# Optimization experiments

Hardware: AMD Instinct MI355X
Metric: run time of the kernel (lower is better)

The kernel has to match this reference:

```python
import jax, jax.numpy as jnp
import numpy as np

B, M, D = 16, 100000, 128
OUT = 128  # out_features; in_features = 2*D


def setup_inputs() -> dict:
    key = jax.random.key(0)
    k1, k2, k3, k4 = jax.random.split(key, 4)
    s1 = 1.0 / np.sqrt(2 * D)  # ~ torch Linear default init scale
    s2 = 1.0 / np.sqrt(OUT)
    return {
        "xx_anchor": jax.random.normal(k1, (B, D), dtype=jnp.float32),
        "input": jax.random.normal(k2, (M, D), dtype=jnp.float32),
        "adj": jnp.zeros((1, 1), dtype=jnp.float32),  # densified then unused in forward math
        "W1": jax.random.normal(k3, (OUT, 2 * D), dtype=jnp.float32) * s1,
        "W2": jax.random.normal(k4, (1, OUT), dtype=jnp.float32) * s2,
    }


def reference(xx_anchor, input, adj, W1, W2):
    d = input.shape[1]
    # concat(q_vec, input) @ W1.T  ==  q @ W1[:, :d].T  +  input @ W1[:, d:].T
    # (avoids materializing the [B, m, 2d] concat tensor; same math)
    anchor_part = xx_anchor @ W1[:, :d].T          # [B, out]
    node_part = input @ W1[:, d:].T                # [m, out]
    h = jax.nn.relu(anchor_part[:, None, :] + node_part[None, :, :])  # [B, m, out]
    scores = jnp.einsum('bmo,o->bm', h, W2[0])     # linear2 -> [B, m]
    atten = jax.nn.softmax(scores, axis=1)          # softmax over node dim
    v_vec = jnp.einsum('bm,md->bd', atten, input)   # weighted sum pooling
    return v_vec
```

## Files before the change

kernel.cpp:

```cpp
#include <hip/hip_runtime.h>
#include <hip/hip_bf16.h>
#include <math.h>


typedef __attribute__((ext_vector_type(8))) short bf16x8;
typedef __attribute__((ext_vector_type(4))) float f32x4;

__device__ __forceinline__ short f2bs(float f) {
    __hip_bfloat16 h = __float2bfloat16(f);
    return *reinterpret_cast<short*>(&h);
}
__device__ __forceinline__ float bs2f(ushort u) {
    union { unsigned int i; float f; } v; v.i = ((unsigned)u) << 16; return v.f;
}

__global__ __launch_bounds__(256) void kA(const float* __restrict__ W1,
                                          const float* __restrict__ xx,
                                          ushort* __restrict__ w1b,
                                          float* __restrict__ A) {
    const int bi = blockIdx.x, t = threadIdx.x;
    if (bi < 64) {
        int idx = bi * 256 + t;
        int o = idx >> 7, d = idx & 127;
        w1b[idx] = (ushort)f2bs(W1[o * 256 + 128 + d]);
        return;
    }
    __shared__ float xxs[16 * 132];
    __shared__ float w1s[16 * 132];
    const int og0 = (bi - 64) * 16;
#pragma unroll
    for (int i = 0; i < 2; ++i) {
        int idx = t + 256 * i;
        int r = idx >> 5, c4 = (idx & 31) << 2;
        *(float4*)&xxs[r * 132 + c4] = *(const float4*)&xx[r * 128 + c4];
        *(float4*)&w1s[r * 132 + c4] = *(const float4*)&W1[(og0 + r) * 256 + c4];
    }
    __syncthreads();
    const int ol = t >> 4, b = t & 15;
    float acc = 0.f;
#pragma unroll
    for (int d4 = 0; d4 < 32; ++d4) {
        float4 xv = *(float4*)&xxs[b * 132 + d4 * 4];
        float4 wv = *(float4*)&w1s[ol * 132 + d4 * 4];
        acc += xv.x * wv.x + xv.y * wv.y + xv.z * wv.z + xv.w * wv.w;
    }
    A[b * 128 + og0 + ol] = acc;
}

__global__ __launch_bounds__(256, 3) void kB(
    const float* __restrict__ in, const ushort* __restrict__ w1b,
    const float* __restrict__ W2, const float* __restrict__ A,
    float* __restrict__ lsum_g, ushort* __restrict__ pacc, int M) {
    __shared__ ushort ins[128 * 136];
    __shared__ float As[16 * 128];
    __shared__ ushort pb[16 * 136];

    const int tid = threadIdx.x, bid = blockIdx.x;
    const int m0 = bid * 128;
    const int w = tid >> 6, lane = tid & 63;
    const int c = lane & 15, q = lane >> 4;
    const int lim = (M - m0 < 128) ? (M - m0) : 128;

#pragma unroll
    for (int i = 0; i < 16; ++i) {
        int idx = tid + 256 * i;
        int r = idx >> 5, c4 = (idx & 31) << 2;
        float4 v = make_float4(0.f, 0.f, 0.f, 0.f);
        if (r < lim) v = *(const float4*)&in[(size_t)(m0 + r) * 128 + c4];
        ushort4 u;
        u.x = (ushort)f2bs(v.x); u.y = (ushort)f2bs(v.y);
        u.z = (ushort)f2bs(v.z); u.w = (ushort)f2bs(v.w);
        *(ushort4*)&ins[r * 136 + c4] = u;
    }
#pragma unroll
    for (int i = 0; i < 2; ++i) {
        int idx = tid + 256 * i;
        *(float4*)&As[idx * 4] = *(const float4*)&A[idx * 4];
    }
    __syncthreads();

    const int mbase = w * 32 + c;
    f32x4 acc[2][8];
#pragma unroll
    for (int mt = 0; mt < 2; ++mt)
#pragma unroll
        for (int ot = 0; ot < 8; ++ot) acc[mt][ot] = (f32x4){0.f, 0.f, 0.f, 0.f};
#pragma unroll
    for (int kb = 0; kb < 4; ++kb) {
        bf16x8 bv0 = *(const bf16x8*)&ins[mbase * 136 + kb * 32 + q * 8];
        bf16x8 bv1 = *(const bf16x8*)&ins[(mbase + 16) * 136 + kb * 32 + q * 8];
#pragma unroll
        for (int ot = 0; ot < 8; ++ot) {
            bf16x8 av = *(const bf16x8*)(w1b + (ot * 16 + c) * 128 + kb * 32 + q * 8);
            acc[0][ot] = __builtin_amdgcn_mfma_f32_16x16x32_bf16(av, bv0, acc[0][ot], 0, 0, 0);
            acc[1][ot] = __builtin_amdgcn_mfma_f32_16x16x32_bf16(av, bv1, acc[1][ot], 0, 0, 0);
        }
    }

    f32x4 w2q[8];
#pragma unroll
    for (int ot = 0; ot < 8; ++ot)
        w2q[ot] = *(const f32x4*)&W2[ot * 16 + q * 4];

    const bool mv0 = (w * 32 + c) < lim;
    const bool mv1 = (w * 32 + 16 + c) < lim;
#pragma unroll
    for (int b = 0; b < 16; ++b) {
        float sa0 = 0.f, sa1 = 0.f;
#pragma unroll
        for (int ot = 0; ot < 8; ++ot) {
            f32x4 aq = *(f32x4*)&As[b * 128 + ot * 16 + q * 4];
#pragma unroll
            for (int r = 0; r < 4; ++r) {
                sa0 += fmaxf(acc[0][ot][r] + aq[r], 0.f) * w2q[ot][r];
                sa1 += fmaxf(acc[1][ot][r] + aq[r], 0.f) * w2q[ot][r];
            }
        }
        sa0 += __shfl_xor(sa0, 16, 64);
        sa0 += __shfl_xor(sa0, 32, 64);
        sa1 += __shfl_xor(sa1, 16, 64);
        sa1 += __shfl_xor(sa1, 32, 64);
        if (q == (b & 3)) {
            pb[b * 136 + w * 32 + c]      = (ushort)f2bs(mv0 ? __expf(sa0) : 0.f);
            pb[b * 136 + w * 32 + 16 + c] = (ushort)f2bs(mv1 ? __expf(sa1) : 0.f);
        }
    }
    __syncthreads();

    f32x4 pd[2];
    pd[0] = (f32x4){0.f, 0.f, 0.f, 0.f};
    pd[1] = (f32x4){0.f, 0.f, 0.f, 0.f};
#pragma unroll
    for (int ks = 0; ks < 4; ++ks) {
        bf16x8 pf = *(const bf16x8*)&pb[c * 136 + ks * 32 + q * 8];
#pragma unroll
        for (int t = 0; t < 2; ++t) {
            const int dloc = w * 32 + t * 16 + c;
            bf16x8 bf;
#pragma unroll
            for (int j = 0; j < 8; ++j)
                bf[j] = (short)ins[(ks * 32 + q * 8 + j) * 136 + dloc];
            pd[t] = __builtin_amdgcn_mfma_f32_16x16x32_bf16(pf, bf, pd[t], 0, 0, 0);
        }
    }
#pragma unroll
    for (int t = 0; t < 2; ++t)
#pragma unroll
        for (int r = 0; r < 4; ++r)
            pacc[((size_t)bid * 16 + q * 4 + r) * 128 + w * 32 + t * 16 + c] =
                (ushort)f2bs(pd[t][r]);

    {
        const int bb = tid >> 4, jj = tid & 15;
        const ushort* pr = &pb[bb * 136 + jj * 8];
        float part = 0.f;
#pragma unroll
        for (int j2 = 0; j2 < 8; ++j2) part += bs2f(pr[j2]);
#pragma unroll
        for (int off = 1; off < 16; off <<= 1) part += __shfl_xor(part, off, 64);
        if (jj == 0) lsum_g[bid * 16 + bb] = part;
    }
}

__global__ __launch_bounds__(256) void kC1(
    const float* __restrict__ lsum_g, const ushort* __restrict__ pacc,
    float* __restrict__ pacc2, float* __restrict__ lsum2, int nb) {
    const int b = blockIdx.x >> 4, s = blockIdx.x & 15;
    const int t = threadIdx.x;
    __shared__ float reda[2 * 128];
    __shared__ float redl[2];
    const int cs = (nb + 15) >> 4;
    const int blk0 = s * cs;
    int blk1 = blk0 + cs; if (blk1 > nb) blk1 = nb;
    const int dd = t & 127, h = t >> 7;
    float ac = 0.f, ls = 0.f;
    for (int blk = blk0 + h; blk < blk1; blk += 2) {
        ac += bs2f(pacc[((size_t)blk * 16 + b) * 128 + dd]);
        ls += lsum_g[blk * 16 + b];
    }
    reda[h * 128 + dd] = ac;
    if (dd == 0) redl[h] = ls;
    __syncthreads();
    if (h == 0) {
        pacc2[((size_t)s * 16 + b) * 128 + dd] = reda[dd] + reda[128 + dd];
        if (dd == 0) lsum2[s * 16 + b] = redl[0] + redl[1];
    }
}

__global__ void kFin(const float* __restrict__ pacc2, const float* __restrict__ lsum2,
                     float* __restrict__ out) {
    const int b = blockIdx.x, t = threadIdx.x;
    float ac = 0.f, ls = 0.f;
#pragma unroll
    for (int s = 0; s < 16; ++s) {
        ac += pacc2[((size_t)s * 16 + b) * 128 + t];
        ls += lsum2[s * 16 + b];
    }
    out[b * 128 + t] = ac / ls;
}

extern "C" void kernel_launch(void* const* d_in, const int* in_sizes, int n_in,
                              void* d_out, int out_size, void* d_ws, size_t ws_size,
                              hipStream_t stream) {
    const float* xx = (const float*)d_in[0];
    const float* in = (const float*)d_in[1];
    const float* W1 = (const float*)d_in[3];
    const float* W2 = (const float*)d_in[4];
    float* out = (float*)d_out;

    const int M = in_sizes[1] / 128;
    const int nb = (M + 127) / 128;

    float* ws = (float*)d_ws;
    float* A      = ws;
    float* lsum_g = A + 2048;
    float* pacc2  = lsum_g + (size_t)nb * 16;
    float* lsum2  = pacc2 + 256 * 128;
    ushort* w1b   = (ushort*)(lsum2 + 256);
    ushort* pacc  = w1b + 16384;

    kA  <<<72, 256, 0, stream>>>(W1, xx, w1b, A);
    kB  <<<nb, 256, 0, stream>>>(in, w1b, W2, A, lsum_g, pacc, M);
    kC1 <<<256, 256, 0, stream>>>(lsum_g, pacc, pacc2, lsum2, nb);
    kFin<<<16, 128, 0, stream>>>(pacc2, lsum2, out);
}
```

Before: 146.3 us.

## Fuse cross-block reduction into main kernel via atomics and last-block finalize

Replaces the per-block bf16 partial outputs and two follow-up reduction kernels with float atomicAdds into a global accumulator, plus a last-block-done counter that writes the final normalized output. It also rewrites relu as 0.5*(x+|x|), hoisting the x*w2 term out of the per-batch loop so the inner loop does abs instead of max. The intent is to cut two kernel launches and the pacc write/read traffic. The cost is heavy atomic contention on 2048 addresses from ~780 blocks, and summation order is no longer deterministic.

```diff
diff --git a/kernel.cpp b/kernel.cpp
--- a/kernel.cpp
+++ b/kernel.cpp
@@ -17,7 +17,10 @@
 __global__ __launch_bounds__(256) void kA(const float* __restrict__ W1,
                                           const float* __restrict__ xx,
                                           ushort* __restrict__ w1b,
-                                          float* __restrict__ A) {
+                                          float* __restrict__ A,
+                                          float* __restrict__ acc_g,
+                                          float* __restrict__ lsum_acc,
+                                          int* __restrict__ counter) {
     const int bi = blockIdx.x, t = threadIdx.x;
     if (bi < 64) {
         int idx = bi * 256 + t;
@@ -25,6 +28,14 @@
         w1b[idx] = (ushort)f2bs(W1[o * 256 + 128 + d]);
         return;
     }
+    if (bi == 72) {
+        for (int i = t; i < 2064; i += 256) {
+            if (i < 2048) acc_g[i] = 0.f;
+            else          lsum_acc[i - 2048] = 0.f;
+        }
+        if (t == 0) *counter = 0;
+        return;
+    }
     __shared__ float xxs[16 * 132];
     __shared__ float w1s[16 * 132];
     const int og0 = (bi - 64) * 16;
@@ -50,7 +61,8 @@
 __global__ __launch_bounds__(256, 3) void kB(
     const float* __restrict__ in, const ushort* __restrict__ w1b,
     const float* __restrict__ W2, const float* __restrict__ A,
-    float* __restrict__ lsum_g, ushort* __restrict__ pacc, int M) {
+    float* __restrict__ acc_g, float* __restrict__ lsum_acc,
+    int* __restrict__ counter, float* __restrict__ out, int M, int nb) {
     __shared__ ushort ins[128 * 136];
     __shared__ float As[16 * 128];
     __shared__ ushort pb[16 * 136];
@@ -99,21 +111,32 @@
 
     f32x4 w2q[8];
 #pragma unroll
+    for (int ot = 0; ot < 8; ++ot) {
+        f32x4 wv = *(const f32x4*)&W2[ot * 16 + q * 4];
+        w2q[ot] = wv * 0.5f;
+    }
+
+    float sm0 = 0.f, sm1 = 0.f;
+#pragma unroll
     for (int ot = 0; ot < 8; ++ot)
-        w2q[ot] = *(const f32x4*)&W2[ot * 16 + q * 4];
+#pragma unroll
+        for (int r = 0; r < 4; ++r) {
+            sm0 += acc[0][ot][r] * w2q[ot][r];
+            sm1 += acc[1][ot][r] * w2q[ot][r];
+        }
 
     const bool mv0 = (w * 32 + c) < lim;
     const bool mv1 = (w * 32 + 16 + c) < lim;
 #pragma unroll
     for (int b = 0; b < 16; ++b) {
-        float sa0 = 0.f, sa1 = 0.f;
+        float sa0 = sm0, sa1 = sm1;
 #pragma unroll
         for (int ot = 0; ot < 8; ++ot) {
             f32x4 aq = *(f32x4*)&As[b * 128 + ot * 16 + q * 4];
 #pragma unroll
             for (int r = 0; r < 4; ++r) {
-                sa0 += fmaxf(acc[0][ot][r] + aq[r], 0.f) * w2q[ot][r];
-                sa1 += fmaxf(acc[1][ot][r] + aq[r], 0.f) * w2q[ot][r];
+                sa0 += fabsf(acc[0][ot][r] + aq[r]) * w2q[ot][r];
+                sa1 += fabsf(acc[1][ot][r] + aq[r]) * w2q[ot][r];
             }
         }
         sa0 += __shfl_xor(sa0, 16, 64);
@@ -147,8 +170,7 @@
     for (int t = 0; t < 2; ++t)
 #pragma unroll
         for (int r = 0; r < 4; ++r)
-            pacc[((size_t)bid * 16 + q * 4 + r) * 128 + w * 32 + t * 16 + c] =
-                (ushort)f2bs(pd[t][r]);
+            atomicAdd(&acc_g[(q * 4 + r) * 128 + w * 32 + t * 16 + c], pd[t][r]);
 
     {
         const int bb = tid >> 4, jj = tid & 15;
@@ -158,45 +180,20 @@
         for (int j2 = 0; j2 < 8; ++j2) part += bs2f(pr[j2]);
 #pragma unroll
         for (int off = 1; off < 16; off <<= 1) part += __shfl_xor(part, off, 64);
-        if (jj == 0) lsum_g[bid * 16 + bb] = part;
-    }
-}
-
-__global__ __launch_bounds__(256) void kC1(
-    const float* __restrict__ lsum_g, const ushort* __restrict__ pacc,
-    float* __restrict__ pacc2, float* __restrict__ lsum2, int nb) {
-    const int b = blockIdx.x >> 4, s = blockIdx.x & 15;
-    const int t = threadIdx.x;
-    __shared__ float reda[2 * 128];
-    __shared__ float redl[2];
-    const int cs = (nb + 15) >> 4;
-    const int blk0 = s * cs;
-    int blk1 = blk0 + cs; if (blk1 > nb) blk1 = nb;
-    const int dd = t & 127, h = t >> 7;
-    float ac = 0.f, ls = 0.f;
-    for (int blk = blk0 + h; blk < blk1; blk += 2) {
-        ac += bs2f(pacc[((size_t)blk * 16 + b) * 128 + dd]);
-        ls += lsum_g[blk * 16 + b];
-    }
-    reda[h * 128 + dd] = ac;
-    if (dd == 0) redl[h] = ls;
-    __syncthreads();
-    if (h == 0) {
-        pacc2[((size_t)s * 16 + b) * 128 + dd] = reda[dd] + reda[128 + dd];
-        if (dd == 0) lsum2[s * 16 + b] = redl[0] + redl[1];
-    }
-}
-
-__global__ void kFin(const float* __restrict__ pacc2, const float* __restrict__ lsum2,
-                     float* __restrict__ out) {
-    const int b = blockIdx.x, t = threadIdx.x;
-    float ac = 0.f, ls = 0.f;
-#pragma unroll
-    for (int s = 0; s < 16; ++s) {
-        ac += pacc2[((size_t)s * 16 + b) * 128 + t];
-        ls += lsum2[s * 16 + b];
-    }
-    out[b * 128 + t] = ac / ls;
+        if (jj == 0) atomicAdd(&lsum_acc[bb], part);
+    }
+
+    __threadfence();
+    __shared__ int isLast;
+    if (tid == 0) isLast = (atomicAdd(counter, 1) == nb - 1);
+    __syncthreads();
+    if (isLast) {
+        for (int i = tid; i < 2048; i += 256) {
+            float a = atomicAdd(&acc_g[i], 0.f);
+            float l = atomicAdd(&lsum_acc[i >> 7], 0.f);
+            out[i] = a / l;
+        }
+    }
 }
 
 extern "C" void kernel_launch(void* const* d_in, const int* in_sizes, int n_in,
@@ -212,15 +209,12 @@
     const int nb = (M + 127) / 128;
 
     float* ws = (float*)d_ws;
-    float* A      = ws;
-    float* lsum_g = A + 2048;
-    float* pacc2  = lsum_g + (size_t)nb * 16;
-    float* lsum2  = pacc2 + 256 * 128;
-    ushort* w1b   = (ushort*)(lsum2 + 256);
-    ushort* pacc  = w1b + 16384;
-
-    kA  <<<72, 256, 0, stream>>>(W1, xx, w1b, A);
-    kB  <<<nb, 256, 0, stream>>>(in, w1b, W2, A, lsum_g, pacc, M);
-    kC1 <<<256, 256, 0, stream>>>(lsum_g, pacc, pacc2, lsum2, nb);
-    kFin<<<16, 128, 0, stream>>>(pacc2, lsum2, out);
-}
+    float* A        = ws;
+    float* acc_g    = ws + 2048;
+    float* lsum_acc = ws + 4096;
+    int*   counter  = (int*)(ws + 4112);
+    ushort* w1b     = (ushort*)(ws + 4116);
+
+    kA <<<73, 256, 0, stream>>>(W1, xx, w1b, A, acc_g, lsum_acc, counter);
+    kB <<<nb, 256, 0, stream>>>(in, w1b, W2, A, acc_g, lsum_acc, counter, out, M, nb);
+}
```

Result: slower. 215.3 us (+47.1%).

## Load input rows directly into MFMA fragments and use abs-based ReLU identity

Applied to the files above, without the earlier changes.

Removes the separate cooperative global-to-LDS staging pass and barrier. Each lane now loads its own input rows from global memory, converts them to bf16 for the MFMA, and also writes them to LDS for the later pooling stage. It also rewrites relu(x)*w as 0.5*w*(x+|x|), hoisting the batch-independent node term out of the 16-batch loop, and splits the accumulators to shorten dependency chains. The cost is less coalesced per-lane global loads (each lane reads a strided 32-byte chunk of a row) and a small change in floating-point rounding.

```diff
diff --git a/kernel.cpp b/kernel.cpp
--- a/kernel.cpp
+++ b/kernel.cpp
@@ -12,6 +12,12 @@
 }
 __device__ __forceinline__ float bs2f(ushort u) {
     union { unsigned int i; float f; } v; v.i = ((unsigned)u) << 16; return v.f;
+}
+__device__ __forceinline__ bf16x8 pack8(float4 a, float4 b) {
+    bf16x8 r;
+    r[0] = f2bs(a.x); r[1] = f2bs(a.y); r[2] = f2bs(a.z); r[3] = f2bs(a.w);
+    r[4] = f2bs(b.x); r[5] = f2bs(b.y); r[6] = f2bs(b.z); r[7] = f2bs(b.w);
+    return r;
 }
 
 __global__ __launch_bounds__(256) void kA(const float* __restrict__ W1,
@@ -62,24 +68,17 @@
     const int lim = (M - m0 < 128) ? (M - m0) : 128;
 
 #pragma unroll
-    for (int i = 0; i < 16; ++i) {
-        int idx = tid + 256 * i;
-        int r = idx >> 5, c4 = (idx & 31) << 2;
-        float4 v = make_float4(0.f, 0.f, 0.f, 0.f);
-        if (r < lim) v = *(const float4*)&in[(size_t)(m0 + r) * 128 + c4];
-        ushort4 u;
-        u.x = (ushort)f2bs(v.x); u.y = (ushort)f2bs(v.y);
-        u.z = (ushort)f2bs(v.z); u.w = (ushort)f2bs(v.w);
-        *(ushort4*)&ins[r * 136 + c4] = u;
-    }
-#pragma unroll
     for (int i = 0; i < 2; ++i) {
         int idx = tid + 256 * i;
         *(float4*)&As[idx * 4] = *(const float4*)&A[idx * 4];
     }
-    __syncthreads();
-
-    const int mbase = w * 32 + c;
+
+    const int r0 = w * 32 + c;
+    const int r1 = r0 + 16;
+    const bool v0 = r0 < lim, v1 = r1 < lim;
+    const float* __restrict__ row0 = in + (size_t)(m0 + r0) * 128;
+    const float* __restrict__ row1 = in + (size_t)(m0 + r1) * 128;
+
     f32x4 acc[2][8];
 #pragma unroll
     for (int mt = 0; mt < 2; ++mt)
@@ -87,11 +86,17 @@
         for (int ot = 0; ot < 8; ++ot) acc[mt][ot] = (f32x4){0.f, 0.f, 0.f, 0.f};
 #pragma unroll
     for (int kb = 0; kb < 4; ++kb) {
-        bf16x8 bv0 = *(const bf16x8*)&ins[mbase * 136 + kb * 32 + q * 8];
-        bf16x8 bv1 = *(const bf16x8*)&ins[(mbase + 16) * 136 + kb * 32 + q * 8];
+        const int k0 = kb * 32 + q * 8;
+        float4 a0 = make_float4(0.f, 0.f, 0.f, 0.f), a1 = a0, b0 = a0, b1 = a0;
+        if (v0) { a0 = *(const float4*)&row0[k0]; a1 = *(const float4*)&row0[k0 + 4]; }
+        if (v1) { b0 = *(const float4*)&row1[k0]; b1 = *(const float4*)&row1[k0 + 4]; }
+        bf16x8 bv0 = pack8(a0, a1);
+        bf16x8 bv1 = pack8(b0, b1);
+        *(bf16x8*)&ins[r0 * 136 + k0] = bv0;
+        *(bf16x8*)&ins[r1 * 136 + k0] = bv1;
 #pragma unroll
         for (int ot = 0; ot < 8; ++ot) {
-            bf16x8 av = *(const bf16x8*)(w1b + (ot * 16 + c) * 128 + kb * 32 + q * 8);
+            bf16x8 av = *(const bf16x8*)(w1b + (ot * 16 + c) * 128 + k0);
             acc[0][ot] = __builtin_amdgcn_mfma_f32_16x16x32_bf16(av, bv0, acc[0][ot], 0, 0, 0);
             acc[1][ot] = __builtin_amdgcn_mfma_f32_16x16x32_bf16(av, bv1, acc[1][ot], 0, 0, 0);
         }
@@ -99,30 +104,44 @@
 
     f32x4 w2q[8];
 #pragma unroll
+    for (int ot = 0; ot < 8; ++ot) {
+        f32x4 wv = *(const f32x4*)&W2[ot * 16 + q * 4];
+        w2q[ot] = wv * 0.5f;
+    }
+    __syncthreads();
+
+    float sm0 = 0.f, sm1 = 0.f;
+#pragma unroll
     for (int ot = 0; ot < 8; ++ot)
-        w2q[ot] = *(const f32x4*)&W2[ot * 16 + q * 4];
-
-    const bool mv0 = (w * 32 + c) < lim;
-    const bool mv1 = (w * 32 + 16 + c) < lim;
+#pragma unroll
+        for (int r = 0; r < 4; ++r) {
+            sm0 += acc[0][ot][r] * w2q[ot][r];
+            sm1 += acc[1][ot][r] * w2q[ot][r];
+        }
+
 #pragma unroll
     for (int b = 0; b < 16; ++b) {
-        float sa0 = 0.f, sa1 = 0.f;
-#pragma unroll
-        for (int ot = 0; ot < 8; ++ot) {
-            f32x4 aq = *(f32x4*)&As[b * 128 + ot * 16 + q * 4];
+        float sa0 = sm0, sa1 = sm1, sb0 = 0.f, sb1 = 0.f;
+#pragma unroll
+        for (int ot = 0; ot < 8; ot += 2) {
+            f32x4 aq0 = *(f32x4*)&As[b * 128 + ot * 16 + q * 4];
+            f32x4 aq1 = *(f32x4*)&As[b * 128 + (ot + 1) * 16 + q * 4];
 #pragma unroll
             for (int r = 0; r < 4; ++r) {
-                sa0 += fmaxf(acc[0][ot][r] + aq[r], 0.f) * w2q[ot][r];
-                sa1 += fmaxf(acc[1][ot][r] + aq[r], 0.f) * w2q[ot][r];
+                sa0 += fabsf(acc[0][ot][r]     + aq0[r]) * w2q[ot][r];
+                sa1 += fabsf(acc[1][ot][r]     + aq0[r]) * w2q[ot][r];
+                sb0 += fabsf(acc[0][ot + 1][r] + aq1[r]) * w2q[ot + 1][r];
+                sb1 += fabsf(acc[1][ot + 1][r] + aq1[r]) * w2q[ot + 1][r];
             }
         }
-        sa0 += __shfl_xor(sa0, 16, 64);
-        sa0 += __shfl_xor(sa0, 32, 64);
-        sa1 += __shfl_xor(sa1, 16, 64);
-        sa1 += __shfl_xor(sa1, 32, 64);
+        float s0 = sa0 + sb0, s1 = sa1 + sb1;
+        s0 += __shfl_xor(s0, 16, 64);
+        s0 += __shfl_xor(s0, 32, 64);
+        s1 += __shfl_xor(s1, 16, 64);
+        s1 += __shfl_xor(s1, 32, 64);
         if (q == (b & 3)) {
-            pb[b * 136 + w * 32 + c]      = (ushort)f2bs(mv0 ? __expf(sa0) : 0.f);
-            pb[b * 136 + w * 32 + 16 + c] = (ushort)f2bs(mv1 ? __expf(sa1) : 0.f);
+            pb[b * 136 + r0] = (ushort)f2bs(v0 ? __expf(s0) : 0.f);
+            pb[b * 136 + r1] = (ushort)f2bs(v1 ? __expf(s1) : 0.f);
         }
     }
     __syncthreads();
```

After: 137.6 us. -6.0%, faster.
